# Kernel optimization log

Hardware: AMD Instinct MI355X
Metric: run time of the kernel (lower is better)

## Reference

```python
import jax, jax.numpy as jnp
import numpy as np

B, LQ, C = 2, 21760, 256
NH, NL, NP = 8, 4, 4
HD = C // NH  # 32
SPATIAL = np.array([[128, 128], [64, 64], [32, 32], [16, 16]], dtype=np.int64)
START = np.array([0, 16384, 20480, 21504], dtype=np.int64)


def setup_inputs() -> dict:
    key = jax.random.key(0)
    ks = jax.random.split(key, 12)
    inp = {
        "query": jax.random.normal(ks[0], (B, LQ, C), jnp.float32),
        "reference_points": jax.random.uniform(ks[1], (B, LQ, NL, 2), jnp.float32),
        "input_flatten": jax.random.normal(ks[2], (B, LQ, C), jnp.float32),
        "input_spatial_shapes": jnp.asarray(SPATIAL),
        "input_level_start_index": jnp.asarray(START),
        # learned params (random small init so offsets stay reasonable)
        "W_off": jax.random.normal(ks[3], (C, NH * NL * NP * 2), jnp.float32) * 0.01,
        "b_off": jax.random.normal(ks[4], (NH * NL * NP * 2,), jnp.float32) * 0.5,
        "W_attn": jax.random.normal(ks[5], (C, NH * NL * NP), jnp.float32) * 0.02,
        "b_attn": jnp.zeros((NH * NL * NP,), jnp.float32),
        "W_val": jax.random.normal(ks[6], (C, C), jnp.float32) * (1.0 / np.sqrt(C)),
        "b_val": jnp.zeros((C,), jnp.float32),
        "W_out": jax.random.normal(ks[7], (C, C), jnp.float32) * (1.0 / np.sqrt(C)),
        "b_out": jnp.zeros((C,), jnp.float32),
    }
    return inp


def _bilinear_sample(v, loc, H, W):
    """v: (BH, H*W, D); loc: (BH, Q, P, 2) in [0,1] (x, y).
    F.grid_sample bilinear, padding_mode='zeros', align_corners=False.
    Returns (BH, Q, P, D)."""
    BH, Q, P, _ = loc.shape
    x = loc[..., 0] * W - 0.5
    y = loc[..., 1] * H - 0.5
    x0 = jnp.floor(x)
    y0 = jnp.floor(y)
    wx1 = x - x0
    wy1 = y - y0

    def corner(xi, yi, w):
        valid = (xi >= 0) & (xi < W) & (yi >= 0) & (yi < H)
        xi_c = jnp.clip(xi, 0, W - 1).astype(jnp.int32)
        yi_c = jnp.clip(yi, 0, H - 1).astype(jnp.int32)
        idx = (yi_c * W + xi_c).reshape(BH, Q * P)
        g = jnp.take_along_axis(v, idx[..., None], axis=1).reshape(BH, Q, P, -1)
        return g * (w * valid)[..., None]

    out = corner(x0, y0, (1.0 - wx1) * (1.0 - wy1))
    out = out + corner(x0 + 1.0, y0, wx1 * (1.0 - wy1))
    out = out + corner(x0, y0 + 1.0, (1.0 - wx1) * wy1)
    out = out + corner(x0 + 1.0, y0 + 1.0, wx1 * wy1)
    return out


def ms_deform_attn(query, reference_points, input_flatten, shapes_np,
                   W_off, b_off, W_attn, b_attn, W_val, b_val, W_out, b_out):
    Bq, Lq, _ = query.shape
    Len_in = input_flatten.shape[1]
    # value projection -> (B*NH, Len_in, HD)
    value = input_flatten @ W_val + b_val
    value = value.reshape(Bq, Len_in, NH, HD).transpose(0, 2, 1, 3).reshape(Bq * NH, Len_in, HD)
    # sampling offsets / attention weights
    offsets = (query @ W_off + b_off).reshape(Bq, Lq, NH, NL, NP, 2)
    attn = jax.nn.softmax((query @ W_attn + b_attn).reshape(Bq, Lq, NH, NL * NP), axis=-1)
    attn = attn.reshape(Bq, Lq, NH, NL, NP)
    # normalizer is (W_l, H_l) per level, matching (x, y) coordinate order
    normalizer = jnp.stack([jnp.asarray(shapes_np[:, 1], jnp.float32),
                            jnp.asarray(shapes_np[:, 0], jnp.float32)], axis=-1)  # (NL, 2)
    loc = reference_points[:, :, None, :, None, :] + offsets / normalizer[None, None, None, :, None, :]
    # (B, Lq, NH, NL, NP, 2) -> (B, NH, Lq, NL, NP, 2) -> (B*NH, Lq, NL, NP, 2)
    loc = loc.transpose(0, 2, 1, 3, 4, 5).reshape(Bq * NH, Lq, NL, NP, 2)
    attn_bh = attn.transpose(0, 2, 1, 3, 4).reshape(Bq * NH, Lq, NL, NP)

    out = jnp.zeros((Bq * NH, Lq, HD), value.dtype)
    start = 0
    for lvl in range(NL):
        Hc, Wc = int(shapes_np[lvl, 0]), int(shapes_np[lvl, 1])
        v_l = value[:, start:start + Hc * Wc]            # (BH, H*W, D)
        samp = _bilinear_sample(v_l, loc[:, :, lvl], Hc, Wc)  # (BH, Lq, P, D)
        out = out + jnp.einsum('bqpd,bqp->bqd', samp, attn_bh[:, :, lvl])
        start += Hc * Wc
    out = out.reshape(Bq, NH, Lq, HD).transpose(0, 2, 1, 3).reshape(Bq, Lq, C)
    return out @ W_out + b_out


def reference(query, reference_points, input_flatten, input_spatial_shapes,
              input_level_start_index, W_off, b_off, W_attn, b_attn,
              W_val, b_val, W_out, b_out):
    shapes_np = np.asarray(input_spatial_shapes)  # static level shapes
    return ms_deform_attn(query, reference_points, input_flatten, shapes_np,
                          W_off, b_off, W_attn, b_attn, W_val, b_val, W_out, b_out)
```

## Files before the change

kernel.cpp:

```cpp
#include <hip/hip_runtime.h>
#include <hip/hip_fp16.h>
#include <type_traits>

#define LQ 21760
#define MROWS 43520
#define LEN 21760

typedef __attribute__((ext_vector_type(8))) _Float16 half8;
typedef __attribute__((ext_vector_type(4))) float f32x4;

__device__ __forceinline__ uint pkh(float a, float b) {
  auto v = __builtin_amdgcn_cvt_pkrtz(a, b);
  return __builtin_bit_cast(uint, v);
}
__device__ __forceinline__ ushort h16(float x) {
  return __half_as_ushort(__float2half(x));
}
__device__ __forceinline__ float hlo(uint u) {
  return __half2float(__ushort_as_half((ushort)(u & 0xffffu)));
}
__device__ __forceinline__ float hhi(uint u) {
  return __half2float(__ushort_as_half((ushort)(u >> 16)));
}

__device__ __forceinline__ int swz8(int row, int k8) {
  return row * 32 + ((k8 ^ (row & 3) ^ ((row >> 2) & 3)) << 3);
}

template <int BN, bool SPLIT, typename AT, typename OT>
__device__ __forceinline__ void gemm_body(
    const AT* __restrict__ A, int lda, const ushort* __restrict__ WT,
    const float* __restrict__ bias, const float* __restrict__ bias2,
    OT* __restrict__ Cout, int ldc, ushort* __restrict__ C2, int mblk,
    ushort* Asb, ushort* Bsb) {
  constexpr int WN = BN / 4;
  constexpr int NI = WN / 16;
  constexpr int BSTEP = (BN * 4) / 512;
  const int tid = threadIdx.x;
  const int m0 = mblk * 128;
  const int w = tid >> 6, wm = w >> 2, wn = w & 3;
  const int l = tid & 63, lr = l & 15, lk = l >> 4;
  const int arow = tid >> 2, ak8 = tid & 3;

  f32x4 acc[4][NI];
#pragma unroll
  for (int mi = 0; mi < 4; ++mi)
#pragma unroll
    for (int ni = 0; ni < NI; ++ni) acc[mi][ni] = {0.f, 0.f, 0.f, 0.f};

  float4 aF0, aF1;
  uint4 aR;
  uint4 bR[BSTEP];

  auto loadA = [&](int k0) {
    const AT* src = A + (size_t)(m0 + arow) * lda + k0 + ak8 * 8;
    if constexpr (std::is_same_v<AT, float>) {
      aF0 = *(const float4*)src;
      aF1 = *(const float4*)(src + 4);
    } else {
      aR = *(const uint4*)src;
    }
  };
  auto loadB = [&](int k0) {
#pragma unroll
    for (int i = 0; i < BSTEP; ++i) {
      int s = tid + i * 512;
      bR[i] = *(const uint4*)(WT + (size_t)(s >> 2) * 256 + k0 + (s & 3) * 8);
    }
  };
  auto writeLDS = [&](int cur) {
    ushort* Ab = Asb + cur * (128 * 32);
    ushort* Bb = Bsb + cur * (BN * 32);
    uint4 pk;
    if constexpr (std::is_same_v<AT, float>)
      pk = make_uint4(pkh(aF0.x, aF0.y), pkh(aF0.z, aF0.w),
                      pkh(aF1.x, aF1.y), pkh(aF1.z, aF1.w));
    else
      pk = aR;
    *(uint4*)&Ab[swz8(arow, ak8)] = pk;
#pragma unroll
    for (int i = 0; i < BSTEP; ++i) {
      int s = tid + i * 512;
      *(uint4*)&Bb[swz8(s >> 2, s & 3)] = bR[i];
    }
  };

  loadA(0);
  loadB(0);
#pragma unroll
  for (int ks = 0; ks < 8; ++ks) {
    const int cur = ks & 1;
    writeLDS(cur);
    __syncthreads();
    if (ks < 7) {
      loadA((ks + 1) * 32);
      loadB((ks + 1) * 32);
    }
    const ushort* Ab = Asb + cur * (128 * 32);
    const ushort* Bb = Bsb + cur * (BN * 32);
    half8 af[4], bfr[NI];
#pragma unroll
    for (int mi = 0; mi < 4; ++mi)
      af[mi] = *(const half8*)&Ab[swz8(wm * 64 + mi * 16 + lr, lk)];
#pragma unroll
    for (int ni = 0; ni < NI; ++ni)
      bfr[ni] = *(const half8*)&Bb[swz8(wn * WN + ni * 16 + lr, lk)];
#pragma unroll
    for (int mi = 0; mi < 4; ++mi)
#pragma unroll
      for (int ni = 0; ni < NI; ++ni)
        acc[mi][ni] = __builtin_amdgcn_mfma_f32_16x16x32_f16(
            af[mi], bfr[ni], acc[mi][ni], 0, 0, 0);
  }
#pragma unroll
  for (int mi = 0; mi < 4; ++mi) {
#pragma unroll
    for (int ni = 0; ni < NI; ++ni) {
      int col = wn * WN + ni * 16 + lr;
      float bs;
      if constexpr (SPLIT)
        bs = (col < 256) ? bias[col] : bias2[col - 256];
      else
        bs = bias[col];
      int row = m0 + wm * 64 + mi * 16 + lk * 4;
#pragma unroll
      for (int r = 0; r < 4; ++r) {
        float v = acc[mi][ni][r] + bs;
        if constexpr (SPLIT) {
          if (col < 256)
            ((ushort*)Cout)[(size_t)(row + r) * 256 + col] = h16(v);
          else
            C2[(size_t)(row + r) * 128 + col - 256] = h16(v);
        } else if constexpr (std::is_same_v<OT, ushort>) {
          Cout[(size_t)(row + r) * ldc + col] = h16(v);
        } else {
          Cout[(size_t)(row + r) * ldc + col] = v;
        }
      }
    }
  }
}

__global__ __launch_bounds__(512) void gemm_front(
    const float* __restrict__ inpf, const ushort* __restrict__ WTv,
    const float* __restrict__ bval, ushort* __restrict__ value16,
    const float* __restrict__ query, const ushort* __restrict__ WTol,
    const float* __restrict__ boff, const float* __restrict__ battn,
    ushort* __restrict__ off16, ushort* __restrict__ logit16) {
  __shared__ ushort Asb[2 * 128 * 32];
  __shared__ ushort Bsb[2 * 384 * 32];
  int bid = blockIdx.x;
  if (bid < 340) {
    gemm_body<256, false, float, ushort>(inpf, 256, WTv, bval, nullptr,
                                         value16, 256, nullptr, bid, Asb, Bsb);
  } else {
    gemm_body<384, true, float, ushort>(query, 256, WTol, boff, battn, off16,
                                        256, logit16, bid - 340, Asb, Bsb);
  }
}

__global__ __launch_bounds__(512) void gemm_out(
    const ushort* __restrict__ midb, const ushort* __restrict__ WTu,
    const float* __restrict__ bout, float* __restrict__ outp) {
  __shared__ ushort Asb[2 * 128 * 32];
  __shared__ ushort Bsb[2 * 256 * 32];
  gemm_body<256, false, ushort, float>(midb, 512, WTu, bout, nullptr, outp,
                                       256, nullptr, blockIdx.x, Asb, Bsb);
}

__global__ __launch_bounds__(256) void wt_cvt_all(
    const float* __restrict__ Wval, const float* __restrict__ Woff,
    const float* __restrict__ Wattn, const float* __restrict__ Wout,
    ushort* __restrict__ WTv, ushort* __restrict__ WTol,
    ushort* __restrict__ WTu) {
  int i = blockIdx.x * 256 + threadIdx.x;
  if (i < 65536) {
    int n = i >> 8, k = i & 255;
    WTv[i] = h16(Wval[(size_t)k * 256 + n]);
  } else if (i < 163840) {
    int j = i - 65536;
    int n = j >> 8, k = j & 255;
    float s = (n < 256) ? Woff[(size_t)k * 256 + n] : Wattn[(size_t)k * 128 + n - 256];
    WTol[j] = h16(s);
  } else {
    int j = i - 163840;
    int n = j >> 8, k = j & 255;
    WTu[j] = h16(Wout[(size_t)k * 256 + n]);
  }
}

__global__ __launch_bounds__(256) void msda_sample(
    const ushort* __restrict__ off16,
    const ushort* __restrict__ logit16,
    const float* __restrict__ refpts,
    const ushort* __restrict__ value,
    ushort* __restrict__ midb) {
  __shared__ float prs[64][16];
  __shared__ float refs[32][4][2];
  __shared__ int tix[1024][4];
  __shared__ uint twp[1024][2];

  const int bid = blockIdx.x;
  const int grp = bid & 7;
  const int sub = bid >> 3;
  const int b = grp >> 2;
  const int hp = grp & 3;
  const int q0 = sub * 32;
  const int tid = threadIdx.x;
  const size_t fqB = (size_t)b * LQ + q0;

  {
    int q = tid >> 3, r = tid & 7;
    refs[q][r >> 1][r & 1] = refpts[(fqB + q) * 8 + r];
  }
  if (tid < 64) {
    int q = tid >> 1, hh = tid & 1;
    int h = hp * 2 + hh;
    const uint4* lp = (const uint4*)(logit16 + (fqB + q) * 128 + h * 16);
    uint4 p0 = lp[0], p1 = lp[1];
    float v[16] = {hlo(p0.x), hhi(p0.x), hlo(p0.y), hhi(p0.y),
                   hlo(p0.z), hhi(p0.z), hlo(p0.w), hhi(p0.w),
                   hlo(p1.x), hhi(p1.x), hlo(p1.y), hhi(p1.y),
                   hlo(p1.z), hhi(p1.z), hlo(p1.w), hhi(p1.w)};
    float m = v[0];
#pragma unroll
    for (int i = 1; i < 16; ++i) m = fmaxf(m, v[i]);
    float s = 0.f;
#pragma unroll
    for (int i = 0; i < 16; ++i) { v[i] = __expf(v[i] - m); s += v[i]; }
    float inv = 1.0f / s;
#pragma unroll
    for (int i = 0; i < 16; ++i) prs[tid][i] = v[i] * inv;
  }
  __syncthreads();

#pragma unroll
  for (int i = 0; i < 4; ++i) {
    int t = tid + i * 256;
    int q = t >> 5;
    int hh = (t >> 4) & 1;
    int lp_ = t & 15;
    int lvl = lp_ >> 2;
    int h = hp * 2 + hh;
    uint op = ((const uint*)off16)[(fqB + q) * 128 + h * 16 + lp_];
    float ox = hlo(op), oy = hhi(op);
    float aw = prs[q * 2 + hh][lp_];
    float rx = refs[q][lvl][0], ry = refs[q][lvl][1];
    int Wl = 128 >> lvl;
    int st = (lvl == 0) ? 0 : ((lvl == 1) ? 16384 : ((lvl == 2) ? 20480 : 21504));
    float fW = (float)Wl;
    float invW = 1.0f / fW;
    float x = (rx + ox * invW) * fW - 0.5f;
    float y = (ry + oy * invW) * fW - 0.5f;
    float x0f = floorf(x), y0f = floorf(y);
    float wx1 = x - x0f, wy1 = y - y0f;
    float wx0 = 1.f - wx1, wy0 = 1.f - wy1;
    int x0 = (int)x0f, y0 = (int)y0f;
    int x1 = x0 + 1, y1 = y0 + 1;
    bool vx0 = (x0 >= 0) & (x0 < Wl), vx1 = (x1 >= 0) & (x1 < Wl);
    bool vy0 = (y0 >= 0) & (y0 < Wl), vy1 = (y1 >= 0) & (y1 < Wl);
    int xc0 = min(max(x0, 0), Wl - 1), xc1 = min(max(x1, 0), Wl - 1);
    int yc0 = min(max(y0, 0), Wl - 1), yc1 = min(max(y1, 0), Wl - 1);
    int base = st * 256 + h * 32;
    int g16 = t >> 4;
    int slot = (t & ~15) | ((t + g16) & 15);
    float w00 = (vx0 && vy0) ? wx0 * wy0 * aw : 0.f;
    float w10 = (vx1 && vy0) ? wx1 * wy0 * aw : 0.f;
    float w01 = (vx0 && vy1) ? wx0 * wy1 * aw : 0.f;
    float w11 = (vx1 && vy1) ? wx1 * wy1 * aw : 0.f;
    tix[slot][0] = base + (yc0 * Wl + xc0) * 256;
    tix[slot][1] = base + (yc0 * Wl + xc1) * 256;
    tix[slot][2] = base + (yc1 * Wl + xc0) * 256;
    tix[slot][3] = base + (yc1 * Wl + xc1) * 256;
    twp[slot][0] = pkh(w00, w10);
    twp[slot][1] = pkh(w01, w11);
  }
  __syncthreads();

  const int g = tid >> 2;
  const int dl = tid & 3;
  const ushort* vb = value + (size_t)b * LEN * 256 + dl * 8;
  float a0 = 0.f, a1 = 0.f, a2 = 0.f, a3 = 0.f;
  float a4 = 0.f, a5 = 0.f, a6 = 0.f, a7 = 0.f;
  uint c0 = 0u, c1 = 0u, c2 = 0u, c3 = 0u;
  const int tb = g * 16;

#define PKC(ACC, U, WP, OS, OSH)                                        \
  asm("v_pk_fma_f16 %0, %1, %2, %0 op_sel:[0," OS ",0] op_sel_hi:[1," OSH \
      ",1]"                                                             \
      : "+v"(ACC)                                                       \
      : "v"(U), "v"(WP))
#define CORNER(U, WPW, OS, OSH)                                         \
  PKC(c0, (U).x, WPW, OS, OSH);                                         \
  PKC(c1, (U).y, WPW, OS, OSH);                                         \
  PKC(c2, (U).z, WPW, OS, OSH);                                         \
  PKC(c3, (U).w, WPW, OS, OSH)
#define PROMO1(ALO, AHI, C)                                             \
  asm("v_fma_mix_f32 %0, 1.0, %1, %0 op_sel:[0,0,0] op_sel_hi:[0,1,0]"  \
      : "+v"(ALO) : "v"(C));                                            \
  asm("v_fma_mix_f32 %0, 1.0, %1, %0 op_sel:[0,1,0] op_sel_hi:[0,1,0]"  \
      : "+v"(AHI) : "v"(C));                                            \
  C = 0u;

#pragma unroll 4
  for (int t = 0; t < 16; ++t) {
    int slot = tb + ((t + g) & 15);
    int4 ix = *(const int4*)&tix[slot][0];
    uint2 wp = *(const uint2*)&twp[slot][0];
    uint4 u0 = *(const uint4*)(vb + ix.x);
    uint4 u1 = *(const uint4*)(vb + ix.y);
    uint4 u2 = *(const uint4*)(vb + ix.z);
    uint4 u3 = *(const uint4*)(vb + ix.w);
    CORNER(u0, wp.x, "0", "0");
    CORNER(u1, wp.x, "1", "1");
    CORNER(u2, wp.y, "0", "0");
    CORNER(u3, wp.y, "1", "1");
    if ((t & 1) == 1) {
      PROMO1(a0, a1, c0);
      PROMO1(a2, a3, c1);
      PROMO1(a4, a5, c2);
      PROMO1(a6, a7, c3);
    }
  }
#undef PROMO1
#undef CORNER
#undef PKC

  const int q = g >> 1, h = hp * 2 + (g & 1);
  ushort* mp = midb + (fqB + q) * 512 + h * 32 + dl * 8;
  *(uint4*)mp = make_uint4(pkh(a0, a1), pkh(a2, a3), pkh(a4, a5), pkh(a6, a7));
}

extern "C" void kernel_launch(void* const* d_in, const int* in_sizes, int n_in,
                              void* d_out, int out_size, void* d_ws,
                              size_t ws_size, hipStream_t stream) {
  (void)in_sizes; (void)n_in; (void)out_size; (void)ws_size;
  const float* query = (const float*)d_in[0];
  const float* refp  = (const float*)d_in[1];
  const float* inpf  = (const float*)d_in[2];
  const float* Woff  = (const float*)d_in[5];
  const float* boff  = (const float*)d_in[6];
  const float* Wattn = (const float*)d_in[7];
  const float* battn = (const float*)d_in[8];
  const float* Wval  = (const float*)d_in[9];
  const float* bval  = (const float*)d_in[10];
  const float* Wout  = (const float*)d_in[11];
  const float* bout  = (const float*)d_in[12];

  ushort* value16 = (ushort*)d_ws;
  ushort* off16   = value16 + (size_t)MROWS * 256;
  ushort* logit16 = off16 + (size_t)MROWS * 256;
  ushort* WTv     = logit16 + (size_t)MROWS * 128;
  ushort* WTol    = WTv + 65536;
  ushort* WTu     = WTol + 98304;

  ushort* midb = (ushort*)d_out;

  wt_cvt_all<<<896, 256, 0, stream>>>(Wval, Woff, Wattn, Wout, WTv, WTol, WTu);

  gemm_front<<<680, 512, 0, stream>>>(inpf, WTv, bval, value16, query, WTol,
                                      boff, battn, off16, logit16);

  msda_sample<<<MROWS / 8, 256, 0, stream>>>(off16, logit16, refp, value16,
                                             midb);

  gemm_out<<<MROWS / 128, 512, 0, stream>>>(midb, WTu, bout, (float*)d_out);
}
```

Measured before the change: 133.2 us.

## Use 64-row tiles for output GEMM and reorder sampling slot traversal

Adds an M-tile parameter to the GEMM body so the output projection runs with 64-row tiles and 8 waves split only along N. This doubles the block count for better CU occupancy, at the cost of less A reuse per block and half the threads idle during A loads. The sampling kernel also changes its LDS slot permutation to an XOR scheme and fully unrolls the 16-point loop in a fixed level-descending order. That order is meant to reduce LDS bank conflicts and change gather locality.

```diff
diff --git a/kernel.cpp b/kernel.cpp
--- a/kernel.cpp
+++ b/kernel.cpp
@@ -27,18 +27,21 @@
   return row * 32 + ((k8 ^ (row & 3) ^ ((row >> 2) & 3)) << 3);
 }
 
-template <int BN, bool SPLIT, typename AT, typename OT>
+template <int BN, int MR, bool SPLIT, typename AT, typename OT>
 __device__ __forceinline__ void gemm_body(
     const AT* __restrict__ A, int lda, const ushort* __restrict__ WT,
     const float* __restrict__ bias, const float* __restrict__ bias2,
     OT* __restrict__ Cout, int ldc, ushort* __restrict__ C2, int mblk,
     ushort* Asb, ushort* Bsb) {
-  constexpr int WN = BN / 4;
+  constexpr int WNW = (MR == 128) ? 4 : 8;
+  constexpr int WN = BN / WNW;
   constexpr int NI = WN / 16;
   constexpr int BSTEP = (BN * 4) / 512;
   const int tid = threadIdx.x;
-  const int m0 = mblk * 128;
-  const int w = tid >> 6, wm = w >> 2, wn = w & 3;
+  const int m0 = mblk * MR;
+  const int w = tid >> 6;
+  const int wm = (MR == 128) ? (w >> 2) : 0;
+  const int wn = (MR == 128) ? (w & 3) : w;
   const int l = tid & 63, lr = l & 15, lk = l >> 4;
   const int arow = tid >> 2, ak8 = tid & 3;
 
@@ -53,6 +56,7 @@
   uint4 bR[BSTEP];
 
   auto loadA = [&](int k0) {
+    if (MR == 64 && tid >= 256) return;
     const AT* src = A + (size_t)(m0 + arow) * lda + k0 + ak8 * 8;
     if constexpr (std::is_same_v<AT, float>) {
       aF0 = *(const float4*)src;
@@ -69,15 +73,17 @@
     }
   };
   auto writeLDS = [&](int cur) {
-    ushort* Ab = Asb + cur * (128 * 32);
+    ushort* Ab = Asb + cur * (MR * 32);
     ushort* Bb = Bsb + cur * (BN * 32);
-    uint4 pk;
-    if constexpr (std::is_same_v<AT, float>)
-      pk = make_uint4(pkh(aF0.x, aF0.y), pkh(aF0.z, aF0.w),
-                      pkh(aF1.x, aF1.y), pkh(aF1.z, aF1.w));
-    else
-      pk = aR;
-    *(uint4*)&Ab[swz8(arow, ak8)] = pk;
+    if (!(MR == 64 && tid >= 256)) {
+      uint4 pk;
+      if constexpr (std::is_same_v<AT, float>)
+        pk = make_uint4(pkh(aF0.x, aF0.y), pkh(aF0.z, aF0.w),
+                        pkh(aF1.x, aF1.y), pkh(aF1.z, aF1.w));
+      else
+        pk = aR;
+      *(uint4*)&Ab[swz8(arow, ak8)] = pk;
+    }
 #pragma unroll
     for (int i = 0; i < BSTEP; ++i) {
       int s = tid + i * 512;
@@ -96,7 +102,7 @@
       loadA((ks + 1) * 32);
       loadB((ks + 1) * 32);
     }
-    const ushort* Ab = Asb + cur * (128 * 32);
+    const ushort* Ab = Asb + cur * (MR * 32);
     const ushort* Bb = Bsb + cur * (BN * 32);
     half8 af[4], bfr[NI];
 #pragma unroll
@@ -151,21 +157,23 @@
   __shared__ ushort Bsb[2 * 384 * 32];
   int bid = blockIdx.x;
   if (bid < 340) {
-    gemm_body<256, false, float, ushort>(inpf, 256, WTv, bval, nullptr,
-                                         value16, 256, nullptr, bid, Asb, Bsb);
+    gemm_body<256, 128, false, float, ushort>(inpf, 256, WTv, bval, nullptr,
+                                              value16, 256, nullptr, bid, Asb,
+                                              Bsb);
   } else {
-    gemm_body<384, true, float, ushort>(query, 256, WTol, boff, battn, off16,
-                                        256, logit16, bid - 340, Asb, Bsb);
+    gemm_body<384, 128, true, float, ushort>(query, 256, WTol, boff, battn,
+                                             off16, 256, logit16, bid - 340,
+                                             Asb, Bsb);
   }
 }
 
 __global__ __launch_bounds__(512) void gemm_out(
     const ushort* __restrict__ midb, const ushort* __restrict__ WTu,
     const float* __restrict__ bout, float* __restrict__ outp) {
-  __shared__ ushort Asb[2 * 128 * 32];
+  __shared__ ushort Asb[2 * 64 * 32];
   __shared__ ushort Bsb[2 * 256 * 32];
-  gemm_body<256, false, ushort, float>(midb, 512, WTu, bout, nullptr, outp,
-                                       256, nullptr, blockIdx.x, Asb, Bsb);
+  gemm_body<256, 64, false, ushort, float>(midb, 512, WTu, bout, nullptr, outp,
+                                           256, nullptr, blockIdx.x, Asb, Bsb);
 }
 
 __global__ __launch_bounds__(256) void wt_cvt_all(
@@ -263,7 +271,7 @@
     int yc0 = min(max(y0, 0), Wl - 1), yc1 = min(max(y1, 0), Wl - 1);
     int base = st * 256 + h * 32;
     int g16 = t >> 4;
-    int slot = (t & ~15) | ((t + g16) & 15);
+    int slot = (t & ~15) | ((lp_ ^ g16) & 15);
     float w00 = (vx0 && vy0) ? wx0 * wy0 * aw : 0.f;
     float w10 = (vx1 && vy0) ? wx1 * wy0 * aw : 0.f;
     float w01 = (vx0 && vy1) ? wx0 * wy1 * aw : 0.f;
@@ -302,9 +310,11 @@
       : "+v"(AHI) : "v"(C));                                            \
   C = 0u;
 
-#pragma unroll 4
+  static constexpr int ORD[16] = {12, 13, 14, 15, 8, 9, 10, 11,
+                                  4,  5,  6,  7,  0, 1, 2,  3};
+#pragma unroll
   for (int t = 0; t < 16; ++t) {
-    int slot = tb + ((t + g) & 15);
+    int slot = tb + ((ORD[t] ^ g) & 15);
     int4 ix = *(const int4*)&tix[slot][0];
     uint2 wp = *(const uint2*)&twp[slot][0];
     uint4 u0 = *(const uint4*)(vb + ix.x);
@@ -364,5 +374,5 @@
   msda_sample<<<MROWS / 8, 256, 0, stream>>>(off16, logit16, refp, value16,
                                              midb);
 
-  gemm_out<<<MROWS / 128, 512, 0, stream>>>(midb, WTu, bout, (float*)d_out);
-}
+  gemm_out<<<MROWS / 64, 512, 0, stream>>>(midb, WTu, bout, (float*)d_out);
+}
```

After: 141.8 us. 6.4% more time.

## Store value head-major and gather adjacent x corners with one contiguous load

Applied to the files above, without the earlier changes.

The value GEMM now writes its output in a per-batch, per-head layout (B*NH, LQ, 32), so each head's pixels are contiguous 64-byte rows. The sampler then fetches the two horizontally adjacent corners as one 128-byte span split across 8 lanes. It stores only a base offset and a y-delta per sample, shifting weights when x0 is negative, and combines the lane halves with a shuffle. This halves the per-sample index and load instruction count and improves gather coalescing. The cost is strided scatter stores in the GEMM epilogue, extra shuffles, and edge-case handling for x at the right border.

```diff
diff --git a/kernel.cpp b/kernel.cpp
--- a/kernel.cpp
+++ b/kernel.cpp
@@ -27,7 +27,7 @@
   return row * 32 + ((k8 ^ (row & 3) ^ ((row >> 2) & 3)) << 3);
 }
 
-template <int BN, bool SPLIT, typename AT, typename OT>
+template <int BN, bool SPLIT, bool VT, typename AT, typename OT>
 __device__ __forceinline__ void gemm_body(
     const AT* __restrict__ A, int lda, const ushort* __restrict__ WT,
     const float* __restrict__ bias, const float* __restrict__ bias2,
@@ -131,6 +131,13 @@
             ((ushort*)Cout)[(size_t)(row + r) * 256 + col] = h16(v);
           else
             C2[(size_t)(row + r) * 128 + col - 256] = h16(v);
+        } else if constexpr (VT) {
+          int rr = row + r;
+          int bb = (rr >= LQ) ? 1 : 0;
+          int pos = rr - bb * LQ;
+          size_t idx =
+              ((size_t)(bb * 8 + (col >> 5)) * LQ + pos) * 32 + (col & 31);
+          ((ushort*)Cout)[idx] = h16(v);
         } else if constexpr (std::is_same_v<OT, ushort>) {
           Cout[(size_t)(row + r) * ldc + col] = h16(v);
         } else {
@@ -151,11 +158,12 @@
   __shared__ ushort Bsb[2 * 384 * 32];
   int bid = blockIdx.x;
   if (bid < 340) {
-    gemm_body<256, false, float, ushort>(inpf, 256, WTv, bval, nullptr,
-                                         value16, 256, nullptr, bid, Asb, Bsb);
+    gemm_body<256, false, true, float, ushort>(
+        inpf, 256, WTv, bval, nullptr, value16, 256, nullptr, bid, Asb, Bsb);
   } else {
-    gemm_body<384, true, float, ushort>(query, 256, WTol, boff, battn, off16,
-                                        256, logit16, bid - 340, Asb, Bsb);
+    gemm_body<384, true, false, float, ushort>(query, 256, WTol, boff, battn,
+                                               off16, 256, logit16, bid - 340,
+                                               Asb, Bsb);
   }
 }
 
@@ -164,8 +172,9 @@
     const float* __restrict__ bout, float* __restrict__ outp) {
   __shared__ ushort Asb[2 * 128 * 32];
   __shared__ ushort Bsb[2 * 256 * 32];
-  gemm_body<256, false, ushort, float>(midb, 512, WTu, bout, nullptr, outp,
-                                       256, nullptr, blockIdx.x, Asb, Bsb);
+  gemm_body<256, false, false, ushort, float>(midb, 512, WTu, bout, nullptr,
+                                              outp, 256, nullptr, blockIdx.x,
+                                              Asb, Bsb);
 }
 
 __global__ __launch_bounds__(256) void wt_cvt_all(
@@ -259,42 +268,35 @@
     int x1 = x0 + 1, y1 = y0 + 1;
     bool vx0 = (x0 >= 0) & (x0 < Wl), vx1 = (x1 >= 0) & (x1 < Wl);
     bool vy0 = (y0 >= 0) & (y0 < Wl), vy1 = (y1 >= 0) & (y1 < Wl);
-    int xc0 = min(max(x0, 0), Wl - 1), xc1 = min(max(x1, 0), Wl - 1);
+    int xc0 = min(max(x0, 0), Wl - 1);
     int yc0 = min(max(y0, 0), Wl - 1), yc1 = min(max(y1, 0), Wl - 1);
-    int base = st * 256 + h * 32;
-    int g16 = t >> 4;
-    int slot = (t & ~15) | ((t + g16) & 15);
     float w00 = (vx0 && vy0) ? wx0 * wy0 * aw : 0.f;
     float w10 = (vx1 && vy0) ? wx1 * wy0 * aw : 0.f;
     float w01 = (vx0 && vy1) ? wx0 * wy1 * aw : 0.f;
     float w11 = (vx1 && vy1) ? wx1 * wy1 * aw : 0.f;
-    tix[slot][0] = base + (yc0 * Wl + xc0) * 256;
-    tix[slot][1] = base + (yc0 * Wl + xc1) * 256;
-    tix[slot][2] = base + (yc1 * Wl + xc0) * 256;
-    tix[slot][3] = base + (yc1 * Wl + xc1) * 256;
-    twp[slot][0] = pkh(w00, w10);
-    twp[slot][1] = pkh(w01, w11);
+    bool xs = (x0 < 0);
+    float lo0 = xs ? w10 : w00, hi0 = xs ? 0.f : w10;
+    float lo1 = xs ? w11 : w01, hi1 = xs ? 0.f : w11;
+    int baseB = (h * LQ + st + yc0 * Wl + xc0) * 64;
+    int dyB = (yc1 - yc0) * Wl * 64;
+    int slot = (t & ~15) | ((lp_ + (t >> 5)) & 15);
+    tix[slot][0] = baseB;
+    tix[slot][1] = dyB;
+    twp[slot][0] = pkh(lo0, hi0);
+    twp[slot][1] = pkh(lo1, hi1);
   }
   __syncthreads();
 
-  const int g = tid >> 2;
-  const int dl = tid & 3;
-  const ushort* vb = value + (size_t)b * LEN * 256 + dl * 8;
-  float a0 = 0.f, a1 = 0.f, a2 = 0.f, a3 = 0.f;
-  float a4 = 0.f, a5 = 0.f, a6 = 0.f, a7 = 0.f;
-  uint c0 = 0u, c1 = 0u, c2 = 0u, c3 = 0u;
-  const int tb = g * 16;
-
-#define PKC(ACC, U, WP, OS, OSH)                                        \
-  asm("v_pk_fma_f16 %0, %1, %2, %0 op_sel:[0," OS ",0] op_sel_hi:[1," OSH \
-      ",1]"                                                             \
+  const int g8 = tid >> 3;
+  const int dl = tid & 7;
+  const uint dlB = (uint)dl * 16u;
+  const uint sh = (uint)((tid & 4) << 2);
+  const char* vb0c = (const char*)(value + (size_t)b * (LEN * 256));
+
+#define PKC(ACC, U, WP)                                                 \
+  asm("v_pk_fma_f16 %0, %1, %2, %0 op_sel:[0,0,0] op_sel_hi:[1,0,1]"    \
       : "+v"(ACC)                                                       \
       : "v"(U), "v"(WP))
-#define CORNER(U, WPW, OS, OSH)                                         \
-  PKC(c0, (U).x, WPW, OS, OSH);                                         \
-  PKC(c1, (U).y, WPW, OS, OSH);                                         \
-  PKC(c2, (U).z, WPW, OS, OSH);                                         \
-  PKC(c3, (U).w, WPW, OS, OSH)
 #define PROMO1(ALO, AHI, C)                                             \
   asm("v_fma_mix_f32 %0, 1.0, %1, %0 op_sel:[0,0,0] op_sel_hi:[0,1,0]"  \
       : "+v"(ALO) : "v"(C));                                            \
@@ -302,33 +304,47 @@
       : "+v"(AHI) : "v"(C));                                            \
   C = 0u;
 
+#pragma unroll
+  for (int half = 0; half < 2; ++half) {
+    const int qh = g8 * 2 + half;
+    const int tb2 = qh * 16;
+    float a0 = 0.f, a1 = 0.f, a2 = 0.f, a3 = 0.f;
+    float a4 = 0.f, a5 = 0.f, a6 = 0.f, a7 = 0.f;
+    uint c0 = 0u, c1 = 0u, c2 = 0u, c3 = 0u;
 #pragma unroll 4
-  for (int t = 0; t < 16; ++t) {
-    int slot = tb + ((t + g) & 15);
-    int4 ix = *(const int4*)&tix[slot][0];
-    uint2 wp = *(const uint2*)&twp[slot][0];
-    uint4 u0 = *(const uint4*)(vb + ix.x);
-    uint4 u1 = *(const uint4*)(vb + ix.y);
-    uint4 u2 = *(const uint4*)(vb + ix.z);
-    uint4 u3 = *(const uint4*)(vb + ix.w);
-    CORNER(u0, wp.x, "0", "0");
-    CORNER(u1, wp.x, "1", "1");
-    CORNER(u2, wp.y, "0", "0");
-    CORNER(u3, wp.y, "1", "1");
-    if ((t & 1) == 1) {
-      PROMO1(a0, a1, c0);
-      PROMO1(a2, a3, c1);
-      PROMO1(a4, a5, c2);
-      PROMO1(a6, a7, c3);
+    for (int t = 0; t < 16; ++t) {
+      int slot = tb2 + ((t + g8) & 15);
+      int2 bx = *(const int2*)&tix[slot][0];
+      uint2 wp = *(const uint2*)&twp[slot][0];
+      const char* p0 = vb0c + (uint)bx.x + dlB;
+      uint4 u0 = *(const uint4*)p0;
+      uint4 u1 = *(const uint4*)(p0 + (uint)bx.y);
+      uint wp0 = wp.x >> sh;
+      uint wp1 = wp.y >> sh;
+      PKC(c0, u0.x, wp0); PKC(c1, u0.y, wp0);
+      PKC(c2, u0.z, wp0); PKC(c3, u0.w, wp0);
+      PKC(c0, u1.x, wp1); PKC(c1, u1.y, wp1);
+      PKC(c2, u1.z, wp1); PKC(c3, u1.w, wp1);
+      if ((t & 3) == 3) {
+        PROMO1(a0, a1, c0);
+        PROMO1(a2, a3, c1);
+        PROMO1(a4, a5, c2);
+        PROMO1(a6, a7, c3);
+      }
+    }
+    a0 += __shfl_xor(a0, 4); a1 += __shfl_xor(a1, 4);
+    a2 += __shfl_xor(a2, 4); a3 += __shfl_xor(a3, 4);
+    a4 += __shfl_xor(a4, 4); a5 += __shfl_xor(a5, 4);
+    a6 += __shfl_xor(a6, 4); a7 += __shfl_xor(a7, 4);
+    if (dl < 4) {
+      const int q = qh >> 1, h = hp * 2 + (qh & 1);
+      ushort* mp = midb + (fqB + q) * 512 + h * 32 + dl * 8;
+      *(uint4*)mp =
+          make_uint4(pkh(a0, a1), pkh(a2, a3), pkh(a4, a5), pkh(a6, a7));
     }
   }
 #undef PROMO1
-#undef CORNER
 #undef PKC
-
-  const int q = g >> 1, h = hp * 2 + (g & 1);
-  ushort* mp = midb + (fqB + q) * 512 + h * 32 + dl * 8;
-  *(uint4*)mp = make_uint4(pkh(a0, a1), pkh(a2, a3), pkh(a4, a5), pkh(a6, a7));
 }
 
 extern "C" void kernel_launch(void* const* d_in, const int* in_sizes, int n_in,
```

New measurement: 128.0 us. 3.9% less time.
